# Kernel optimization log

Measured on AMD Instinct MI355X. Metric: run time of the kernel, lower is better.

## Reference

```python
import jax, jax.numpy as jnp
import numpy as np
import math

H = 16          # num heads
D = 64          # head dim
MAX_POS = 512   # max_position_embeddings


def setup_inputs() -> dict:
    key = jax.random.key(0)
    ks = jax.random.split(key, 8)
    B, S, E = 8, 512, 1024
    scale = 1.0 / math.sqrt(E)
    return {
        "hidden_states": jax.random.normal(ks[0], (B, S, E), jnp.float32),
        "attention_mask": jnp.zeros((B, 1, 1, S), jnp.float32),
        "Wq": jax.random.normal(ks[1], (E, E), jnp.float32) * scale,
        "bq": jnp.zeros((E,), jnp.float32),
        "Wk": jax.random.normal(ks[2], (E, E), jnp.float32) * scale,
        "bk": jnp.zeros((E,), jnp.float32),
        "Wv": jax.random.normal(ks[3], (E, E), jnp.float32) * scale,
        "bv": jnp.zeros((E,), jnp.float32),
        "dist_emb": jax.random.normal(ks[4], (2 * MAX_POS - 1, D), jnp.float32) * 0.02,
    }


def reference(hidden_states, attention_mask, Wq, bq, Wk, bk, Wv, bv, dist_emb):
    B, S, E = hidden_states.shape

    def heads(x):  # [B,S,E] -> [B,H,S,D]
        return x.reshape(B, S, H, D).transpose(0, 2, 1, 3)

    q = heads(hidden_states @ Wq + bq)
    k = heads(hidden_states @ Wk + bk)
    v = heads(hidden_states @ Wv + bv)

    # raw scores [B,H,S,S]
    scores = jnp.einsum('bhld,bhrd->bhlr', q, k)

    # relative position embedding lookup: distance[l,r] = l - r
    pos = jnp.arange(S)
    distance = pos[:, None] - pos[None, :]               # [S,S]
    pe = dist_emb[distance + MAX_POS - 1]                # [S,S,D]
    scores = scores + jnp.einsum('bhld,lrd->bhlr', q, pe)
    scores = scores + jnp.einsum('bhrd,lrd->bhlr', k, pe)

    scores = scores / math.sqrt(D) + attention_mask
    probs = jax.nn.softmax(scores, axis=-1)

    ctx = jnp.einsum('bhlr,bhrd->bhld', probs, v)        # [B,H,S,D]
    ctx = ctx.transpose(0, 2, 1, 3).reshape(B, S, H * D)
    return ctx
```

## Files before the change

### kernel.cpp

```cpp
#include <hip/hip_runtime.h>

#define BATCH 8
#define SEQ   512
#define EMB   1024
#define NH    16
#define HD    64

typedef __bf16 bf16x8 __attribute__((ext_vector_type(8)));
typedef float  f32x4  __attribute__((ext_vector_type(4)));

__device__ __forceinline__ unsigned short f2bf(float f){
  union { float f; unsigned u; } v; v.f = f;
  unsigned r = v.u + 0x7FFFu + ((v.u >> 16) & 1u);
  return (unsigned short)(r >> 16);
}
__device__ __forceinline__ unsigned short f2bfr(float f){
  union { float f; unsigned u; } v; v.f = f;
  return (unsigned short)((v.u + 0x8000u) >> 16);
}
__device__ __forceinline__ float bf2f(unsigned short s){
  union { unsigned u; float f; } v; v.u = ((unsigned)s) << 16;
  return v.f;
}

__device__ __forceinline__ float dpp_max16(float x){
  int t;
  t = __builtin_amdgcn_update_dpp(0, __builtin_bit_cast(int, x), 0xB1, 0xF, 0xF, true);
  x = fmaxf(x, __builtin_bit_cast(float, t));
  t = __builtin_amdgcn_update_dpp(0, __builtin_bit_cast(int, x), 0x4E, 0xF, 0xF, true);
  x = fmaxf(x, __builtin_bit_cast(float, t));
  t = __builtin_amdgcn_update_dpp(0, __builtin_bit_cast(int, x), 0x141, 0xF, 0xF, true);
  x = fmaxf(x, __builtin_bit_cast(float, t));
  t = __builtin_amdgcn_update_dpp(0, __builtin_bit_cast(int, x), 0x140, 0xF, 0xF, true);
  x = fmaxf(x, __builtin_bit_cast(float, t));
  return x;
}
__device__ __forceinline__ float dpp_sum16(float x){
  int t;
  t = __builtin_amdgcn_update_dpp(0, __builtin_bit_cast(int, x), 0xB1, 0xF, 0xF, true);
  x += __builtin_bit_cast(float, t);
  t = __builtin_amdgcn_update_dpp(0, __builtin_bit_cast(int, x), 0x4E, 0xF, 0xF, true);
  x += __builtin_bit_cast(float, t);
  t = __builtin_amdgcn_update_dpp(0, __builtin_bit_cast(int, x), 0x141, 0xF, 0xF, true);
  x += __builtin_bit_cast(float, t);
  t = __builtin_amdgcn_update_dpp(0, __builtin_bit_cast(int, x), 0x140, 0xF, 0xF, true);
  x += __builtin_bit_cast(float, t);
  return x;
}

__device__ __forceinline__ int swzc(int row, int chunk){
  return row * 128 + (((chunk ^ (row & 7)) & 7) << 4);
}
__device__ __forceinline__ int swz2(int row, int col){
  return row * 128 + ((((col >> 3) ^ (row & 7)) & 7) << 4) + ((col & 7) << 1);
}

__device__ __forceinline__ void gload16(const unsigned short* g, unsigned char* lds){
  __builtin_amdgcn_global_load_lds((const __attribute__((address_space(1))) unsigned int*)g,
                                   (__attribute__((address_space(3))) unsigned int*)lds,
                                   16, 0, 0);
}

__device__ __forceinline__ void bar_lds(){
  asm volatile("s_waitcnt lgkmcnt(0)" ::: "memory");
  __builtin_amdgcn_s_barrier();
}

__global__ void k_pre(const float* __restrict__ hid, unsigned short* __restrict__ hidb,
                      const float* __restrict__ dist, unsigned short* __restrict__ distb,
                      const float* __restrict__ Wq, const float* __restrict__ Wk,
                      const float* __restrict__ Wv, unsigned short* __restrict__ wqt,
                      unsigned short* __restrict__ wkt, unsigned short* __restrict__ wvt){
  int bid = blockIdx.x;
  int t = threadIdx.x;
  if (bid < 4096){
    int i = (bid * 256 + t) * 4;
    float4 v = *(const float4*)(hid + i);
    ushort4 o; o.x = f2bf(v.x); o.y = f2bf(v.y); o.z = f2bf(v.z); o.w = f2bf(v.w);
    *(ushort4*)(hidb + i) = o;
  } else if (bid < 4352){
    int i = (bid - 4096) * 256 + t;
    distb[i] = (i < 1023 * 64) ? f2bf(dist[i]) : (unsigned short)0;
  } else {
    int wt = bid - 4352;
    int z = wt >> 10, rem = wt & 1023;
    const float* W = (z == 0) ? Wq : (z == 1) ? Wk : Wv;
    unsigned short* WT = (z == 0) ? wqt : (z == 1) ? wkt : wvt;
    __shared__ float tl[32][33];
    int n0 = (rem & 31) * 32, k0 = (rem >> 5) * 32;
    int tx = t & 31, ty = t >> 5;
#pragma unroll
    for (int i = 0; i < 4; i++)
      tl[ty + 8*i][tx] = W[(k0 + ty + 8*i) * EMB + n0 + tx];
    __syncthreads();
#pragma unroll
    for (int i = 0; i < 4; i++)
      WT[(n0 + ty + 8*i) * EMB + k0 + tx] = f2bf(tl[tx][ty + 8*i]);
  }
}

__global__ __launch_bounds__(256, 3) void k_gemm3(const unsigned short* __restrict__ A,
                                                  const unsigned short* __restrict__ wqt,
                                                  const unsigned short* __restrict__ wkt,
                                                  const unsigned short* __restrict__ wvt,
                                                  const float* __restrict__ bq,
                                                  const float* __restrict__ bk,
                                                  const float* __restrict__ bv,
                                                  unsigned short* __restrict__ qb,
                                                  unsigned short* __restrict__ kb,
                                                  unsigned short* __restrict__ vtb){
  int z = blockIdx.z;
  const unsigned short* BT = (z == 0) ? wqt : (z == 1) ? wkt : wvt;
  const float* bias = (z == 0) ? bq : (z == 1) ? bk : bv;
  unsigned short* out = (z == 0) ? qb : (z == 1) ? kb : vtb;
  int mode = (z == 2);

  __shared__ __align__(16) unsigned char sA[128 * 128];
  __shared__ __align__(16) unsigned char sB[128 * 128];
  int m0 = blockIdx.y * 128, n0 = blockIdx.x * 128;
  int t = threadIdx.x, w = t >> 6, lane = t & 63, g = lane >> 4, lr = lane & 15;
  int rowbase = (w >> 1) * 64, colbase = (w & 1) * 64;
  int lrow = lane >> 3, lc = lane & 7;
  f32x4 acc[4][4] = {};
  for (int k0 = 0; k0 < EMB; k0 += 64){
    __syncthreads();
#pragma unroll
    for (int i = 0; i < 4; i++){
      int row = (w + 4*i) * 8 + lrow;
      int cg  = lc ^ (row & 7);
      gload16(A  + (m0 + row) * EMB + k0 + cg*8, sA + (w + 4*i) * 1024);
      gload16(BT + (n0 + row) * EMB + k0 + cg*8, sB + (w + 4*i) * 1024);
    }
    __syncthreads();
#pragma unroll
    for (int kk = 0; kk < 2; kk++){
      bf16x8 af[4], bfv[4];
#pragma unroll
      for (int i = 0; i < 4; i++) af[i]  = *(const bf16x8*)(sA + swzc(rowbase + 16*i + lr, kk*4 + g));
#pragma unroll
      for (int j = 0; j < 4; j++) bfv[j] = *(const bf16x8*)(sB + swzc(colbase + 16*j + lr, kk*4 + g));
#pragma unroll
      for (int i = 0; i < 4; i++)
#pragma unroll
        for (int j = 0; j < 4; j++)
          acc[i][j] = __builtin_amdgcn_mfma_f32_16x16x32_bf16(af[i], bfv[j], acc[i][j], 0, 0, 0);
    }
  }
#pragma unroll
  for (int i = 0; i < 4; i++)
#pragma unroll
    for (int j = 0; j < 4; j++)
#pragma unroll
      for (int r = 0; r < 4; r++){
        int m = m0 + rowbase + 16*i + 4*g + r;
        int n = n0 + colbase + 16*j + lr;
        float val = acc[i][j][r] + bias[n];
        int b = m >> 9, s = m & 511, h = n >> 6, d = n & 63;
        int idx = (mode == 0) ? (((b*NH + h)*SEQ + s)*HD + d)
                              : (((b*NH + h)*HD + d)*SEQ + s);
        out[idx] = f2bf(val);
      }
}

__global__ __launch_bounds__(256, 2) void k_attn(const unsigned short* __restrict__ qb,
                                                 const unsigned short* __restrict__ kb,
                                                 const unsigned short* __restrict__ vtb,
                                                 const unsigned short* __restrict__ distb,
                                                 const float* __restrict__ mask,
                                                 float* __restrict__ out){
  __shared__ __align__(16) unsigned char sK[64 * 128];
  __shared__ __align__(16) unsigned char sV[64 * 128];
  __shared__ __align__(16) unsigned char sSA[4][2624];
  __shared__ __align__(16) unsigned char sSB[4][2560];

  const float SCL  = 0.125f * 1.4426950408889634f;
  const float L2E  = 1.4426950408889634f;

  int bid = blockIdx.x;
  int wgid = (bid & 7) * 128 + (bid >> 3);
  int lt = wgid & 7, h = (wgid >> 3) & 15, b = wgid >> 7;
  int L0 = lt * 64;
  int bh = b * NH + h;
  int t = threadIdx.x, w = t >> 6, lane = t & 63, g = lane >> 4, lr = lane & 15;
  int lbase = 16 * w;
  unsigned char* mySA = sSA[w];
  unsigned char* mySB = sSB[w];
  unsigned char* myP  = mySA;
  const float* maskp = mask + b * SEQ;

  const unsigned short* qrow = qb + (bh * SEQ + L0 + lbase + lr) * HD + 8 * g;
  bf16x8 aq0 = *(const bf16x8*)qrow;
  bf16x8 aq1 = *(const bf16x8*)(qrow + 32);

  bf16x8 pe[5][2];
#define LOAD_PE(JB) do {                                                     \
    const unsigned short* _pb = distb + ((JB) + 16*w + lr) * HD + 8*g;       \
    _Pragma("unroll")                                                        \
    for (int _j = 0; _j < 5; _j++){                                          \
      pe[_j][0] = *(const bf16x8*)(_pb + _j*16*HD);                          \
      pe[_j][1] = *(const bf16x8*)(_pb + _j*16*HD + 32); }                   \
  } while(0)

  int lrow = lane >> 3, lc = lane & 7;
  int row0 = w * 8 + lrow,      row1 = (w + 4) * 8 + lrow;
  int cg0  = lc ^ (row0 & 7),   cg1  = lc ^ (row1 & 7);
  const unsigned short* kbase = kb  + bh * SEQ * HD;
  const unsigned short* vbase = vtb + bh * HD * SEQ;

  uint4 kst0 = *(const uint4*)(kbase + row0 * HD  + cg0 * 8);
  uint4 kst1 = *(const uint4*)(kbase + row1 * HD  + cg1 * 8);
  uint4 vst0 = *(const uint4*)(vbase + row0 * SEQ + cg0 * 8);
  uint4 vst1 = *(const uint4*)(vbase + row1 * SEQ + cg1 * 8);
  LOAD_PE(L0 + 448);

  f32x4 o[4] = {};
  float mrun[4], srun[4];
#pragma unroll
  for (int r = 0; r < 4; r++){ mrun[r] = -1e30f; srun[r] = 0.f; }

  for (int rt = 0; rt < 8; rt++){
    int R0 = rt * 64;

    float mreg[4];
#pragma unroll
    for (int f = 0; f < 4; f++) mreg[f] = maskp[R0 + 16*f + lr];

    __builtin_amdgcn_s_setprio(1);
#pragma unroll
    for (int jt2 = 0; jt2 < 5; jt2++){
      f32x4 a = {};
      a = __builtin_amdgcn_mfma_f32_16x16x32_bf16(aq0, pe[jt2][0], a, 0, 0, 0);
      a = __builtin_amdgcn_mfma_f32_16x16x32_bf16(aq1, pe[jt2][1], a, 0, 0, 0);
#pragma unroll
      for (int reg = 0; reg < 4; reg++){
        int rloc = 63 + 4*g + reg - lr - 16*jt2;
        int addr = ((unsigned)rloc < 64u) ? (rloc*40 + (4*g + reg)*2) : 2560;
        *(unsigned short*)(mySA + addr) = f2bfr(a[reg]);
      }
    }
    __builtin_amdgcn_s_setprio(0);

    bar_lds();

    *(uint4*)(sK + w * 1024 + lane * 16)       = kst0;
    *(uint4*)(sK + (w + 4) * 1024 + lane * 16) = kst1;
    *(uint4*)(sV + w * 1024 + lane * 16)       = vst0;
    *(uint4*)(sV + (w + 4) * 1024 + lane * 16) = vst1;

    if (rt < 7){
      const unsigned short* ks = kbase + (R0 + 64) * HD;
      const unsigned short* vs = vbase + (R0 + 64);
      kst0 = *(const uint4*)(ks + row0 * HD  + cg0 * 8);
      kst1 = *(const uint4*)(ks + row1 * HD  + cg1 * 8);
      vst0 = *(const uint4*)(vs + row0 * SEQ + cg0 * 8);
      vst1 = *(const uint4*)(vs + row1 * SEQ + cg1 * 8);
    }

    bar_lds();

    __builtin_amdgcn_s_setprio(1);
    f32x4 sc[4];
#pragma unroll
    for (int f = 0; f < 4; f++){
      bf16x8 k0 = *(const bf16x8*)(sK + swzc(16*f + lr, g));
      bf16x8 k1 = *(const bf16x8*)(sK + swzc(16*f + lr, 4 + g));
      f32x4 a = {};
      a = __builtin_amdgcn_mfma_f32_16x16x32_bf16(aq0, k0, a, 0, 0, 0);
      a = __builtin_amdgcn_mfma_f32_16x16x32_bf16(aq1, k1, a, 0, 0, 0);
      sc[f] = a;
      f32x4 b0 = {}, b1 = {};
      b0 = __builtin_amdgcn_mfma_f32_16x16x32_bf16(k0, pe[3 - f][0], b0, 0, 0, 0);
      b0 = __builtin_amdgcn_mfma_f32_16x16x32_bf16(k1, pe[3 - f][1], b0, 0, 0, 0);
      b1 = __builtin_amdgcn_mfma_f32_16x16x32_bf16(k0, pe[4 - f][0], b1, 0, 0, 0);
      b1 = __builtin_amdgcn_mfma_f32_16x16x32_bf16(k1, pe[4 - f][1], b1, 0, 0, 0);
#pragma unroll
      for (int reg = 0; reg < 4; reg++){
        int ss = 4*g + reg + lr;
        float v = (ss >= 15) ? b0[reg] : b1[reg];
        int row = 16*f + 4*g + reg;
        int col = (ss + 1) & 15;
        *(unsigned short*)(mySB + row*40 + col*2) = f2bfr(v);
      }
    }
    __builtin_amdgcn_s_setprio(0);

    if (rt < 7) LOAD_PE(L0 + 448 - 64*(rt + 1));

#pragma unroll
    for (int f = 0; f < 4; f++){
      ushort4 sa = *(const ushort4*)(mySA + (16*f + lr)*40 + 8*g);
      ushort4 sb = *(const ushort4*)(mySB + (16*f + lr)*40 + 8*g);
      float madd = mreg[f] * L2E;
      sc[f][0] = (sc[f][0] + bf2f(sa.x) + bf2f(sb.x)) * SCL + madd;
      sc[f][1] = (sc[f][1] + bf2f(sa.y) + bf2f(sb.y)) * SCL + madd;
      sc[f][2] = (sc[f][2] + bf2f(sa.z) + bf2f(sb.z)) * SCL + madd;
      sc[f][3] = (sc[f][3] + bf2f(sa.w) + bf2f(sb.w)) * SCL + madd;
    }

    float tm[4];
    bool sml = true;
#pragma unroll
    for (int r = 0; r < 4; r++){
      float t0 = fmaxf(fmaxf(sc[0][r], sc[1][r]), fmaxf(sc[2][r], sc[3][r]));
      tm[r] = dpp_max16(t0);
      sml = sml && (tm[r] - mrun[r] <= 8.0f);
    }
    if (__all(sml)){
#pragma unroll
      for (int r = 0; r < 4; r++){
        float ps = 0.f;
#pragma unroll
        for (int f = 0; f < 4; f++){ float p = exp2f(sc[f][r] - mrun[r]); sc[f][r] = p; ps += p; }
        ps = dpp_sum16(ps);
        srun[r] += ps;
      }
    } else {
#pragma unroll
      for (int r = 0; r < 4; r++){
        float mnew = fmaxf(mrun[r], tm[r]);
        float fr = exp2f(mrun[r] - mnew);
        float ps = 0.f;
#pragma unroll
        for (int f = 0; f < 4; f++){ float p = exp2f(sc[f][r] - mnew); sc[f][r] = p; ps += p; }
        ps = dpp_sum16(ps);
        srun[r] = srun[r] * fr + ps;
        mrun[r] = mnew;
#pragma unroll
        for (int df = 0; df < 4; df++) o[df][r] *= fr;
      }
    }

#pragma unroll
    for (int f = 0; f < 4; f++)
#pragma unroll
      for (int r = 0; r < 4; r++)
        *(unsigned short*)(myP + swz2(4*g + r, 16*f + lr)) = f2bfr(sc[f][r]);

    __builtin_amdgcn_s_setprio(1);
#pragma unroll
    for (int kk = 0; kk < 2; kk++){
      bf16x8 pf = *(const bf16x8*)(myP + swzc(lr, kk*4 + g));
#pragma unroll
      for (int df = 0; df < 4; df++){
        bf16x8 vf = *(const bf16x8*)(sV + swzc(16*df + lr, kk*4 + g));
        o[df] = __builtin_amdgcn_mfma_f32_16x16x32_bf16(pf, vf, o[df], 0, 0, 0);
      }
    }
    __builtin_amdgcn_s_setprio(0);
  }

#pragma unroll
  for (int r = 0; r < 4; r++){
    float inv = 1.0f / srun[r];
#pragma unroll
    for (int df = 0; df < 4; df++){
      int l = L0 + lbase + 4*g + r;
      out[(b * SEQ + l) * EMB + h * HD + 16*df + lr] = o[df][r] * inv;
    }
  }
#undef LOAD_PE
}

extern "C" void kernel_launch(void* const* d_in, const int* in_sizes, int n_in,
                              void* d_out, int out_size, void* d_ws, size_t ws_size,
                              hipStream_t stream) {
  (void)in_sizes; (void)n_in; (void)out_size; (void)ws_size;
  const float* hid  = (const float*)d_in[0];
  const float* mask = (const float*)d_in[1];
  const float* Wq   = (const float*)d_in[2];
  const float* bq   = (const float*)d_in[3];
  const float* Wk   = (const float*)d_in[4];
  const float* bk   = (const float*)d_in[5];
  const float* Wv   = (const float*)d_in[6];
  const float* bv   = (const float*)d_in[7];
  const float* dist = (const float*)d_in[8];
  float* out = (float*)d_out;

  unsigned char* ws = (unsigned char*)d_ws;
  unsigned short* hidb  = (unsigned short*)ws;
  unsigned short* wqt   = hidb + 4096 * 1024;
  unsigned short* wkt   = wqt  + 1024 * 1024;
  unsigned short* wvt   = wkt  + 1024 * 1024;
  unsigned short* distb = wvt  + 1024 * 1024;
  unsigned short* qb    = distb + 1024 * 64;
  unsigned short* kb    = qb + BATCH * NH * SEQ * HD;
  unsigned short* vtb   = kb + BATCH * NH * SEQ * HD;

  k_pre<<<7424, 256, 0, stream>>>(hid, hidb, dist, distb, Wq, Wk, Wv, wqt, wkt, wvt);
  k_gemm3<<<dim3(8, 32, 3), 256, 0, stream>>>(hidb, wqt, wkt, wvt, bq, bk, bv, qb, kb, vtb);
  k_attn<<<1024, 256, 0, stream>>>(qb, kb, vtb, distb, mask, out);
}
```

Baseline: 110.4 us.

## Double attention query tile to 128 rows with 8 waves and native bf16 conversion

The attention kernel now runs 512-thread blocks, each covering 128 query rows. That halves the grid and halves the K/V tile loads per query row, since each wave stages only one K row-group and one V row-group. The q·pe relative-position product is moved after the barrier and the k·pe loop, so both run inside the same high-priority MFMA region. Manual float-to-bf16 bit tricks are replaced by native __bf16 casts, which changes rounding to round-to-nearest-even and may map to hardware conversion instructions. The tighter launch bounds (512 threads, 2 blocks) reduce the register budget per thread, which risks spills or lower scheduling flexibility.

```diff
diff --git a/kernel.cpp b/kernel.cpp
--- a/kernel.cpp
+++ b/kernel.cpp
@@ -10,13 +10,7 @@
 typedef float  f32x4  __attribute__((ext_vector_type(4)));
 
 __device__ __forceinline__ unsigned short f2bf(float f){
-  union { float f; unsigned u; } v; v.f = f;
-  unsigned r = v.u + 0x7FFFu + ((v.u >> 16) & 1u);
-  return (unsigned short)(r >> 16);
-}
-__device__ __forceinline__ unsigned short f2bfr(float f){
-  union { float f; unsigned u; } v; v.f = f;
-  return (unsigned short)((v.u + 0x8000u) >> 16);
+  return __builtin_bit_cast(unsigned short, (__bf16)f);
 }
 __device__ __forceinline__ float bf2f(unsigned short s){
   union { unsigned u; float f; } v; v.u = ((unsigned)s) << 16;
@@ -162,7 +156,7 @@
       }
 }
 
-__global__ __launch_bounds__(256, 2) void k_attn(const unsigned short* __restrict__ qb,
+__global__ __launch_bounds__(512, 2) void k_attn(const unsigned short* __restrict__ qb,
                                                  const unsigned short* __restrict__ kb,
                                                  const unsigned short* __restrict__ vtb,
                                                  const unsigned short* __restrict__ distb,
@@ -170,16 +164,16 @@
                                                  float* __restrict__ out){
   __shared__ __align__(16) unsigned char sK[64 * 128];
   __shared__ __align__(16) unsigned char sV[64 * 128];
-  __shared__ __align__(16) unsigned char sSA[4][2624];
-  __shared__ __align__(16) unsigned char sSB[4][2560];
+  __shared__ __align__(16) unsigned char sSA[8][2624];
+  __shared__ __align__(16) unsigned char sSB[8][2560];
 
   const float SCL  = 0.125f * 1.4426950408889634f;
   const float L2E  = 1.4426950408889634f;
 
   int bid = blockIdx.x;
-  int wgid = (bid & 7) * 128 + (bid >> 3);
-  int lt = wgid & 7, h = (wgid >> 3) & 15, b = wgid >> 7;
-  int L0 = lt * 64;
+  int wgid = (bid & 7) * 64 + (bid >> 3);
+  int lt = wgid & 3, h = (wgid >> 2) & 15, b = wgid >> 6;
+  int L0 = lt * 128;
   int bh = b * NH + h;
   int t = threadIdx.x, w = t >> 6, lane = t & 63, g = lane >> 4, lr = lane & 15;
   int lbase = 16 * w;
@@ -202,15 +196,13 @@
   } while(0)
 
   int lrow = lane >> 3, lc = lane & 7;
-  int row0 = w * 8 + lrow,      row1 = (w + 4) * 8 + lrow;
-  int cg0  = lc ^ (row0 & 7),   cg1  = lc ^ (row1 & 7);
+  int row0 = w * 8 + lrow;
+  int cg0  = lc ^ (row0 & 7);
   const unsigned short* kbase = kb  + bh * SEQ * HD;
   const unsigned short* vbase = vtb + bh * HD * SEQ;
 
   uint4 kst0 = *(const uint4*)(kbase + row0 * HD  + cg0 * 8);
-  uint4 kst1 = *(const uint4*)(kbase + row1 * HD  + cg1 * 8);
   uint4 vst0 = *(const uint4*)(vbase + row0 * SEQ + cg0 * 8);
-  uint4 vst1 = *(const uint4*)(vbase + row1 * SEQ + cg1 * 8);
   LOAD_PE(L0 + 448);
 
   f32x4 o[4] = {};
@@ -221,40 +213,19 @@
   for (int rt = 0; rt < 8; rt++){
     int R0 = rt * 64;
 
+    bar_lds();
+
+    *(uint4*)(sK + w * 1024 + lane * 16) = kst0;
+    *(uint4*)(sV + w * 1024 + lane * 16) = vst0;
+
+    if (rt < 7){
+      kst0 = *(const uint4*)(kbase + (R0 + 64) * HD + row0 * HD  + cg0 * 8);
+      vst0 = *(const uint4*)(vbase + (R0 + 64)      + row0 * SEQ + cg0 * 8);
+    }
+
     float mreg[4];
 #pragma unroll
     for (int f = 0; f < 4; f++) mreg[f] = maskp[R0 + 16*f + lr];
-
-    __builtin_amdgcn_s_setprio(1);
-#pragma unroll
-    for (int jt2 = 0; jt2 < 5; jt2++){
-      f32x4 a = {};
-      a = __builtin_amdgcn_mfma_f32_16x16x32_bf16(aq0, pe[jt2][0], a, 0, 0, 0);
-      a = __builtin_amdgcn_mfma_f32_16x16x32_bf16(aq1, pe[jt2][1], a, 0, 0, 0);
-#pragma unroll
-      for (int reg = 0; reg < 4; reg++){
-        int rloc = 63 + 4*g + reg - lr - 16*jt2;
-        int addr = ((unsigned)rloc < 64u) ? (rloc*40 + (4*g + reg)*2) : 2560;
-        *(unsigned short*)(mySA + addr) = f2bfr(a[reg]);
-      }
-    }
-    __builtin_amdgcn_s_setprio(0);
-
-    bar_lds();
-
-    *(uint4*)(sK + w * 1024 + lane * 16)       = kst0;
-    *(uint4*)(sK + (w + 4) * 1024 + lane * 16) = kst1;
-    *(uint4*)(sV + w * 1024 + lane * 16)       = vst0;
-    *(uint4*)(sV + (w + 4) * 1024 + lane * 16) = vst1;
-
-    if (rt < 7){
-      const unsigned short* ks = kbase + (R0 + 64) * HD;
-      const unsigned short* vs = vbase + (R0 + 64);
-      kst0 = *(const uint4*)(ks + row0 * HD  + cg0 * 8);
-      kst1 = *(const uint4*)(ks + row1 * HD  + cg1 * 8);
-      vst0 = *(const uint4*)(vs + row0 * SEQ + cg0 * 8);
-      vst1 = *(const uint4*)(vs + row1 * SEQ + cg1 * 8);
-    }
 
     bar_lds();
 
@@ -279,7 +250,20 @@
         float v = (ss >= 15) ? b0[reg] : b1[reg];
         int row = 16*f + 4*g + reg;
         int col = (ss + 1) & 15;
-        *(unsigned short*)(mySB + row*40 + col*2) = f2bfr(v);
+        *(__bf16*)(mySB + row*40 + col*2) = (__bf16)v;
+      }
+    }
+
+#pragma unroll
+    for (int jt2 = 0; jt2 < 5; jt2++){
+      f32x4 a = {};
+      a = __builtin_amdgcn_mfma_f32_16x16x32_bf16(aq0, pe[jt2][0], a, 0, 0, 0);
+      a = __builtin_amdgcn_mfma_f32_16x16x32_bf16(aq1, pe[jt2][1], a, 0, 0, 0);
+#pragma unroll
+      for (int reg = 0; reg < 4; reg++){
+        int rloc = 63 + 4*g + reg - lr - 16*jt2;
+        int addr = ((unsigned)rloc < 64u) ? (rloc*40 + (4*g + reg)*2) : 2560;
+        *(__bf16*)(mySA + addr) = (__bf16)a[reg];
       }
     }
     __builtin_amdgcn_s_setprio(0);
@@ -334,7 +318,7 @@
     for (int f = 0; f < 4; f++)
 #pragma unroll
       for (int r = 0; r < 4; r++)
-        *(unsigned short*)(myP + swz2(4*g + r, 16*f + lr)) = f2bfr(sc[f][r]);
+        *(__bf16*)(myP + swz2(4*g + r, 16*f + lr)) = (__bf16)sc[f][r];
 
     __builtin_amdgcn_s_setprio(1);
 #pragma unroll
@@ -388,5 +372,5 @@
 
   k_pre<<<7424, 256, 0, stream>>>(hid, hidb, dist, distb, Wq, Wk, Wv, wqt, wkt, wvt);
   k_gemm3<<<dim3(8, 32, 3), 256, 0, stream>>>(hidb, wqt, wkt, wvt, bq, bk, bv, qb, kb, vtb);
-  k_attn<<<1024, 256, 0, stream>>>(qb, kb, vtb, distb, mask, out);
-}
+  k_attn<<<512, 512, 0, stream>>>(qb, kb, vtb, distb, mask, out);
+}
```

Measured after the change: 104.1 us. -5.7%, faster.
